# Performance work log

Measured on AMD Instinct MI355X. Metric: run time of the kernel, lower is better.

## Reference

```python
import jax, jax.numpy as jnp
import numpy as np

TEMPERATURE = 0.07
BASE_TEMPERATURE = 0.07


def setup_inputs() -> dict:
    key = jax.random.key(0)
    k1, k2 = jax.random.split(key)
    N, D = 8192, 512
    features = jax.random.normal(k1, (N, D), dtype=jnp.float32)
    labels = jax.random.randint(k2, (N,), 0, 64, dtype=jnp.int64 if jax.config.jax_enable_x64 else jnp.int32)
    return {"features": features, "labels": labels, "rotation_multiplier": 2}


def reference(features, labels, rotation_multiplier):
    k = int(rotation_multiplier)
    N = features.shape[0]
    B = N // k
    # L2-normalize rows (torch F.normalize clamps norm at eps=1e-12)
    norm = jnp.maximum(jnp.linalg.norm(features, axis=1, keepdims=True), 1e-12)
    f = features / norm
    sim = jnp.matmul(f, f.T) / TEMPERATURE  # [N, N]

    # block positive mask: groups of k rows share a label; compare group labels
    lab = labels.reshape(B, k)[:, 0]  # [B]
    same = lab[:, None] == lab[None, :]  # [B, B]
    mask = jnp.repeat(jnp.repeat(same, k, axis=0), k, axis=1)  # [N, N]
    eye = jnp.eye(N, dtype=bool)
    mask = mask & ~eye

    # stable masked log-softmax with diagonal removed from denominator
    logits_max = jax.lax.stop_gradient(jnp.max(sim, axis=1, keepdims=True))
    logits = sim - logits_max
    exp_logits = jnp.exp(logits)
    denom = exp_logits.sum(axis=1, keepdims=True) - jnp.diagonal(exp_logits)[:, None] + 1e-8
    log_prob = logits - jnp.log(denom)

    mask_f = mask.astype(logits.dtype)
    mask_sum = mask_f.sum(axis=1)  # [N]
    valid = mask_sum > 0
    mean_log_prob_pos = (log_prob * mask_f).sum(axis=1) / jnp.maximum(mask_sum, 1.0)
    per_sample = -(TEMPERATURE / BASE_TEMPERATURE) * mean_log_prob_pos
    n_valid = valid.sum().astype(logits.dtype)
    loss = jnp.where(valid, per_sample, 0.0).sum() / jnp.maximum(n_valid, 1.0)
    return loss
```

## Files before the change

kernel.cpp:

```cpp
#include <hip/hip_runtime.h>
#include <hip/hip_bf16.h>

#define TEMP_INV 14.285714285714286f
#define FSCALE 16.0f
#define T1S (TEMP_INV / 256.0f)

typedef __attribute__((ext_vector_type(4))) float f32x4;
typedef __attribute__((ext_vector_type(4))) int i32x4;
typedef __attribute__((ext_vector_type(8))) int i32x8;

#define ASYNC_COPY16(gp, lp)                                                  \
  __builtin_amdgcn_global_load_lds(                                          \
      (__attribute__((address_space(1))) const void*)(gp),                    \
      (__attribute__((address_space(3))) void*)(lp), 16, 0, 0)

__global__ __launch_bounds__(256) void norm_label_k(const float* __restrict__ feat,
                                                    uchar* __restrict__ fq,
                                                    const int* __restrict__ labels,
                                                    const int* __restrict__ kptr,
                                                    int* __restrict__ glab,
                                                    int* __restrict__ cnt,
                                                    float* __restrict__ gacc,
                                                    int* __restrict__ dcnt,
                                                    int N, int D) {
  const int row = (blockIdx.x * 256 + threadIdx.x) >> 6;
  const int lane = threadIdx.x & 63;
  if (row < N) {
    const float4* fr = (const float4*)(feat + (size_t)row * D);
    float4 v0 = fr[lane * 2];
    float4 v1 = fr[lane * 2 + 1];
    float ss = v0.x * v0.x + v0.y * v0.y + v0.z * v0.z + v0.w * v0.w +
               v1.x * v1.x + v1.y * v1.y + v1.z * v1.z + v1.w * v1.w;
    #pragma unroll
    for (int off = 32; off; off >>= 1) ss += __shfl_xor(ss, off, 64);
    const float inv = FSCALE / fmaxf(sqrtf(ss), 1e-12f);
    int w0 = 0, w1 = 0;
    w0 = __builtin_amdgcn_cvt_pk_fp8_f32(v0.x * inv, v0.y * inv, w0, false);
    w0 = __builtin_amdgcn_cvt_pk_fp8_f32(v0.z * inv, v0.w * inv, w0, true);
    w1 = __builtin_amdgcn_cvt_pk_fp8_f32(v1.x * inv, v1.y * inv, w1, false);
    w1 = __builtin_amdgcn_cvt_pk_fp8_f32(v1.z * inv, v1.w * inv, w1, true);
    uint2 o; o.x = (uint)w0; o.y = (uint)w1;
    const int pofs = (lane >> 4) * 128 + (lane & 3) * 32 + ((lane >> 2) & 3) * 8;
    *(uint2*)(fq + (size_t)row * D + pofs) = o;
  }
  if (blockIdx.x == 0) {
    const int k = *kptr;
    const int B = N / k;
    __shared__ int h[64];
    const int t = threadIdx.x;
    if (t < 2) gacc[t] = 0.f;
    if (t == 2) *dcnt = 0;
    if (t < 64) h[t] = 0;
    __syncthreads();
    for (int b = t; b < B; b += 256) {
      int lb = labels[(size_t)b * k];
      if (lb >= 0 && lb < 64) atomicAdd(&h[lb], 1);
    }
    __syncthreads();
    if (t < 64) cnt[t] = h[t];
    for (int i = t; i < N; i += 256) glab[i] = labels[(size_t)(i / k) * k];
  }
}

__global__ __launch_bounds__(256, 4) void gemm_k(const uchar* __restrict__ fq,
                                                 const int* __restrict__ glab,
                                                 float* __restrict__ part,
                                                 int N, int D) {
  __shared__ uchar As[128 * 128];
  __shared__ uchar Bs[128 * 128];
  const int t = threadIdx.x;
  const int lane = t & 63;
  const int wid = t >> 6;
  const int wrow = wid >> 1, wcol = wid & 1;
  const int quad = lane >> 4, l15 = lane & 15;

  const int nb = N / 128;
  const int total = nb * (nb + 1) / 2;
  int gidx = blockIdx.x;
  if ((total & 7) == 0) {
    const int per = total >> 3;
    gidx = (blockIdx.x & 7) * per + (blockIdx.x >> 3);
  }
  int idx = gidx, bi = 0;
  while (idx >= nb - bi) { idx -= nb - bi; bi++; }
  const int bj = bi + idx;
  const int i0 = bi * 128, j0 = bj * 128;
  const bool diagblk = (bi == bj);

  f32x4 acc[4][4];
  #pragma unroll
  for (int mi = 0; mi < 4; mi++)
    #pragma unroll
    for (int ni = 0; ni < 4; ni++) {
      f32x4 z = {0.f, 0.f, 0.f, 0.f};
      acc[mi][ni] = z;
    }

  uchar* sb = (wid < 2) ? As : Bs;
  const int rbase = (wid & 1) * 64;
  const int rowstart = ((wid < 2) ? i0 : j0) + rbase;
  const int lrow = lane >> 3;
  const int lch = lane & 7;

  for (int kb = 0; kb < D; kb += 128) {
    __syncthreads();
    #pragma unroll
    for (int i = 0; i < 8; i++) {
      const int rl = 8 * i + lrow;
      const int cg = lch ^ (rl & 7);
      ASYNC_COPY16(fq + (size_t)(rowstart + rl) * D + kb + cg * 16,
                   sb + (rbase + 8 * i) * 128);
    }
    __syncthreads();
    i32x8 av[4];
    #pragma unroll
    for (int mi = 0; mi < 4; mi++) {
      const int r = wrow * 64 + mi * 16 + l15;
      i32x4 lo = *(const i32x4*)&As[r * 128 + (((2 * quad) ^ (r & 7)) << 4)];
      i32x4 hi = *(const i32x4*)&As[r * 128 + (((2 * quad + 1) ^ (r & 7)) << 4)];
      av[mi] = (i32x8){lo.x, lo.y, lo.z, lo.w, hi.x, hi.y, hi.z, hi.w};
    }
    #pragma unroll
    for (int ni = 0; ni < 4; ni++) {
      const int r = wcol * 64 + ni * 16 + l15;
      i32x4 lo = *(const i32x4*)&Bs[r * 128 + (((2 * quad) ^ (r & 7)) << 4)];
      i32x4 hi = *(const i32x4*)&Bs[r * 128 + (((2 * quad + 1) ^ (r & 7)) << 4)];
      i32x8 bv = (i32x8){lo.x, lo.y, lo.z, lo.w, hi.x, hi.y, hi.z, hi.w};
      #pragma unroll
      for (int mi = 0; mi < 4; mi++)
        acc[mi][ni] = __builtin_amdgcn_mfma_scale_f32_16x16x128_f8f6f4(
            av[mi], bv, acc[mi][ni], 0, 0, 0, 127, 0, 127);
    }
  }

  __syncthreads();
  float* sf = (float*)As;
  const int colbase = j0 + wcol * 64 + l15;
  int clab[4];
  #pragma unroll
  for (int ni = 0; ni < 4; ni++) clab[ni] = glab[colbase + ni * 16];

  float colE[4] = {0.f, 0.f, 0.f, 0.f};
  float colP[4] = {0.f, 0.f, 0.f, 0.f};

  #pragma unroll
  for (int mi = 0; mi < 4; mi++) {
    const int lrw = wrow * 64 + mi * 16 + quad * 4;
    #pragma unroll
    for (int r = 0; r < 4; r++) {
      const int row = i0 + lrw + r;
      const int rlab = glab[row];
      float Ssum = 0.f, Psum = 0.f;
      #pragma unroll
      for (int ni = 0; ni < 4; ni++) {
        const int col = colbase + ni * 16;
        const float val = acc[mi][ni][r];
        const float lg = fmaf(val, T1S, -TEMP_INV);
        const bool diag = diagblk && (row == col);
        const float e = diag ? 0.f : __expf(lg);
        const float pm = (!diag && rlab == clab[ni]) ? lg : 0.f;
        Ssum += e; Psum += pm;
        colE[ni] += e; colP[ni] += pm;
      }
      #pragma unroll
      for (int off = 8; off; off >>= 1) {
        Ssum += __shfl_xor(Ssum, off, 64);
        Psum += __shfl_xor(Psum, off, 64);
      }
      if (l15 == 0) {
        sf[wcol * 128 + lrw + r]       = Ssum;
        sf[256 + wcol * 128 + lrw + r] = Psum;
      }
    }
  }
  if (!diagblk) {
    #pragma unroll
    for (int ni = 0; ni < 4; ni++) {
      float e = colE[ni];
      float p = colP[ni];
      e += __shfl_xor(e, 16, 64);
      e += __shfl_xor(e, 32, 64);
      p += __shfl_xor(p, 16, 64);
      p += __shfl_xor(p, 32, 64);
      const int lcol = wcol * 64 + ni * 16 + l15;
      if (quad == 0) {
        sf[512 + wrow * 128 + lcol] = e;
        sf[768 + wrow * 128 + lcol] = p;
      }
    }
  }
  __syncthreads();
  float* dst = part + (size_t)gidx * 512;
  if (t < 128) {
    dst[t]       = sf[t] + sf[128 + t];
    dst[128 + t] = sf[256 + t] + sf[384 + t];
  } else if (!diagblk) {
    const int u = t - 128;
    dst[256 + u] = sf[512 + u] + sf[640 + u];
    dst[384 + u] = sf[768 + u] + sf[896 + u];
  }
}

__global__ __launch_bounds__(512) void reduce_loss_k(const float* __restrict__ part,
                                                     const int* __restrict__ glab,
                                                     const int* __restrict__ cnt,
                                                     const int* __restrict__ kptr,
                                                     float* __restrict__ gacc,
                                                     int* __restrict__ dcnt,
                                                     float* __restrict__ out, int N) {
  const int nb = N / 128;
  const int b = blockIdx.x;
  const int t = threadIdx.x & 127;
  const int sl = threadIdx.x >> 7;
  float S = 0.f, P = 0.f;
  const int base = b * nb - b * (b - 1) / 2;
  for (int bj = b + sl; bj < nb; bj += 4) {
    const float* p = part + (size_t)(base + bj - b) * 512;
    S += p[t];
    P += p[128 + t];
  }
  for (int bi = sl; bi < b; bi += 4) {
    const int idx = bi * nb - bi * (bi - 1) / 2 + (b - bi);
    const float* p = part + (size_t)idx * 512;
    S += p[256 + t];
    P += p[384 + t];
  }
  __shared__ float sS[4][128], sP[4][128];
  sS[sl][t] = S; sP[sl][t] = P;
  __syncthreads();
  float l = 0.f, v = 0.f;
  if (sl == 0) {
    S = sS[0][t] + sS[1][t] + sS[2][t] + sS[3][t];
    P = sP[0][t] + sP[1][t] + sP[2][t] + sP[3][t];
    const int k = *kptr;
    const int np = cnt[glab[b * 128 + t]] * k - 1;
    if (np > 0) {
      l = -(P - (float)np * logf(S + 1e-8f)) / (float)np;
      v = 1.f;
    }
  }
  #pragma unroll
  for (int off = 32; off; off >>= 1) {
    l += __shfl_xor(l, off, 64);
    v += __shfl_xor(v, off, 64);
  }
  __shared__ float sl8[8], sv8[8];
  const int tt = threadIdx.x;
  if ((tt & 63) == 0) { sl8[tt >> 6] = l; sv8[tt >> 6] = v; }
  __syncthreads();
  if (tt == 0) {
    float L = 0.f, V = 0.f;
    #pragma unroll
    for (int i = 0; i < 8; i++) { L += sl8[i]; V += sv8[i]; }
    atomicAdd(&gacc[0], L);
    atomicAdd(&gacc[1], V);
    __threadfence();
    const int prev = atomicAdd(dcnt, 1);
    if (prev == (int)gridDim.x - 1) {
      const float Lf = atomicAdd(&gacc[0], 0.f);
      const float Vf = atomicAdd(&gacc[1], 0.f);
      out[0] = Lf / fmaxf(Vf, 1.f);
    }
  }
}

extern "C" void kernel_launch(void* const* d_in, const int* in_sizes, int n_in,
                              void* d_out, int out_size, void* d_ws, size_t ws_size,
                              hipStream_t stream) {
  const float* feat = (const float*)d_in[0];
  const int* labels = (const int*)d_in[1];
  const int* kptr   = (const int*)d_in[2];
  const int N = in_sizes[1];
  const int D = in_sizes[0] / N;

  const int nb = N / 128;
  const int total = nb * (nb + 1) / 2;

  char* ws = (char*)d_ws;
  uchar* fq = (uchar*)ws;
  size_t off = (size_t)N * D;
  float* part = (float*)(ws + off); off += (size_t)total * 512 * sizeof(float);
  int* glab   = (int*)(ws + off);   off += (size_t)N * sizeof(int);
  int* cnt    = (int*)(ws + off);   off += 64 * sizeof(int);
  float* gacc = (float*)(ws + off); off += 2 * sizeof(float);
  int* dcnt   = (int*)(ws + off);   off += sizeof(int);

  norm_label_k<<<(N + 3) / 4, 256, 0, stream>>>(feat, fq, labels, kptr, glab, cnt,
                                                gacc, dcnt, N, D);
  gemm_k<<<total, 256, 0, stream>>>(fq, glab, part, N, D);
  reduce_loss_k<<<nb, 512, 0, stream>>>(part, glab, cnt, kptr, gacc, dcnt,
                                        (float*)d_out, N);
}
```

Before: 135.8 us.

## Move label histogram into reduce kernel and widen reduce blocks

Block 0 of the normalize kernel no longer serially computes the label histogram and the full group-label array. Each row's group label is now written by its own wave, and the 64-bin histogram is recomputed per block inside the reduce kernel in shared memory. The reduce kernel also grows to 1024 threads with 8 slices over the partial tiles. This removes a straggler block from the first kernel at the cost of redundant histogram work in every reduce block.

```diff
diff --git a/kernel.cpp b/kernel.cpp
--- a/kernel.cpp
+++ b/kernel.cpp
@@ -14,15 +14,14 @@
       (__attribute__((address_space(1))) const void*)(gp),                    \
       (__attribute__((address_space(3))) void*)(lp), 16, 0, 0)
 
-__global__ __launch_bounds__(256) void norm_label_k(const float* __restrict__ feat,
-                                                    uchar* __restrict__ fq,
-                                                    const int* __restrict__ labels,
-                                                    const int* __restrict__ kptr,
-                                                    int* __restrict__ glab,
-                                                    int* __restrict__ cnt,
-                                                    float* __restrict__ gacc,
-                                                    int* __restrict__ dcnt,
-                                                    int N, int D) {
+__global__ __launch_bounds__(256) void norm_k(const float* __restrict__ feat,
+                                              uchar* __restrict__ fq,
+                                              const int* __restrict__ labels,
+                                              const int* __restrict__ kptr,
+                                              int* __restrict__ glab,
+                                              float* __restrict__ gacc,
+                                              int* __restrict__ dcnt,
+                                              int N, int D) {
   const int row = (blockIdx.x * 256 + threadIdx.x) >> 6;
   const int lane = threadIdx.x & 63;
   if (row < N) {
@@ -42,23 +41,14 @@
     uint2 o; o.x = (uint)w0; o.y = (uint)w1;
     const int pofs = (lane >> 4) * 128 + (lane & 3) * 32 + ((lane >> 2) & 3) * 8;
     *(uint2*)(fq + (size_t)row * D + pofs) = o;
-  }
-  if (blockIdx.x == 0) {
-    const int k = *kptr;
-    const int B = N / k;
-    __shared__ int h[64];
-    const int t = threadIdx.x;
-    if (t < 2) gacc[t] = 0.f;
-    if (t == 2) *dcnt = 0;
-    if (t < 64) h[t] = 0;
-    __syncthreads();
-    for (int b = t; b < B; b += 256) {
-      int lb = labels[(size_t)b * k];
-      if (lb >= 0 && lb < 64) atomicAdd(&h[lb], 1);
-    }
-    __syncthreads();
-    if (t < 64) cnt[t] = h[t];
-    for (int i = t; i < N; i += 256) glab[i] = labels[(size_t)(i / k) * k];
+    if (lane == 0) {
+      const int k = *kptr;
+      glab[row] = labels[(size_t)(row / k) * k];
+    }
+  }
+  if (blockIdx.x == 0 && threadIdx.x < 3) {
+    if (threadIdx.x < 2) gacc[threadIdx.x] = 0.f;
+    else *dcnt = 0;
   }
 }
 
@@ -201,39 +191,51 @@
   }
 }
 
-__global__ __launch_bounds__(512) void reduce_loss_k(const float* __restrict__ part,
-                                                     const int* __restrict__ glab,
-                                                     const int* __restrict__ cnt,
-                                                     const int* __restrict__ kptr,
-                                                     float* __restrict__ gacc,
-                                                     int* __restrict__ dcnt,
-                                                     float* __restrict__ out, int N) {
+__global__ __launch_bounds__(1024) void reduce_loss_k(const float* __restrict__ part,
+                                                      const int* __restrict__ glab,
+                                                      const int* __restrict__ labels,
+                                                      const int* __restrict__ kptr,
+                                                      float* __restrict__ gacc,
+                                                      int* __restrict__ dcnt,
+                                                      float* __restrict__ out, int N) {
   const int nb = N / 128;
   const int b = blockIdx.x;
-  const int t = threadIdx.x & 127;
-  const int sl = threadIdx.x >> 7;
+  const int tt = threadIdx.x;
+  const int t = tt & 127;
+  const int sl = tt >> 7;
+  const int k = *kptr;
+  const int B = N / k;
+
+  __shared__ int h[64];
+  if (tt < 64) h[tt] = 0;
+  __syncthreads();
+  for (int g = tt; g < B; g += 1024) {
+    int lb = labels[(size_t)g * k];
+    if (lb >= 0 && lb < 64) atomicAdd(&h[lb], 1);
+  }
+
   float S = 0.f, P = 0.f;
   const int base = b * nb - b * (b - 1) / 2;
-  for (int bj = b + sl; bj < nb; bj += 4) {
+  for (int bj = b + sl; bj < nb; bj += 8) {
     const float* p = part + (size_t)(base + bj - b) * 512;
     S += p[t];
     P += p[128 + t];
   }
-  for (int bi = sl; bi < b; bi += 4) {
+  for (int bi = sl; bi < b; bi += 8) {
     const int idx = bi * nb - bi * (bi - 1) / 2 + (b - bi);
     const float* p = part + (size_t)idx * 512;
     S += p[256 + t];
     P += p[384 + t];
   }
-  __shared__ float sS[4][128], sP[4][128];
+  __shared__ float sS[8][128], sP[8][128];
   sS[sl][t] = S; sP[sl][t] = P;
   __syncthreads();
   float l = 0.f, v = 0.f;
   if (sl == 0) {
-    S = sS[0][t] + sS[1][t] + sS[2][t] + sS[3][t];
-    P = sP[0][t] + sP[1][t] + sP[2][t] + sP[3][t];
-    const int k = *kptr;
-    const int np = cnt[glab[b * 128 + t]] * k - 1;
+    S = 0.f; P = 0.f;
+    #pragma unroll
+    for (int s = 0; s < 8; s++) { S += sS[s][t]; P += sP[s][t]; }
+    const int np = h[glab[b * 128 + t]] * k - 1;
     if (np > 0) {
       l = -(P - (float)np * logf(S + 1e-8f)) / (float)np;
       v = 1.f;
@@ -244,14 +246,13 @@
     l += __shfl_xor(l, off, 64);
     v += __shfl_xor(v, off, 64);
   }
-  __shared__ float sl8[8], sv8[8];
-  const int tt = threadIdx.x;
-  if ((tt & 63) == 0) { sl8[tt >> 6] = l; sv8[tt >> 6] = v; }
+  __shared__ float sl16[16], sv16[16];
+  if ((tt & 63) == 0) { sl16[tt >> 6] = l; sv16[tt >> 6] = v; }
   __syncthreads();
   if (tt == 0) {
     float L = 0.f, V = 0.f;
     #pragma unroll
-    for (int i = 0; i < 8; i++) { L += sl8[i]; V += sv8[i]; }
+    for (int i = 0; i < 16; i++) { L += sl16[i]; V += sv16[i]; }
     atomicAdd(&gacc[0], L);
     atomicAdd(&gacc[1], V);
     __threadfence();
@@ -281,13 +282,12 @@
   size_t off = (size_t)N * D;
   float* part = (float*)(ws + off); off += (size_t)total * 512 * sizeof(float);
   int* glab   = (int*)(ws + off);   off += (size_t)N * sizeof(int);
-  int* cnt    = (int*)(ws + off);   off += 64 * sizeof(int);
   float* gacc = (float*)(ws + off); off += 2 * sizeof(float);
   int* dcnt   = (int*)(ws + off);   off += sizeof(int);
 
-  norm_label_k<<<(N + 3) / 4, 256, 0, stream>>>(feat, fq, labels, kptr, glab, cnt,
-                                                gacc, dcnt, N, D);
+  norm_k<<<(N + 3) / 4, 256, 0, stream>>>(feat, fq, labels, kptr, glab,
+                                          gacc, dcnt, N, D);
   gemm_k<<<total, 256, 0, stream>>>(fq, glab, part, N, D);
-  reduce_loss_k<<<nb, 512, 0, stream>>>(part, glab, cnt, kptr, gacc, dcnt,
-                                        (float*)d_out, N);
-}
+  reduce_loss_k<<<nb, 1024, 0, stream>>>(part, glab, labels, kptr, gacc, dcnt,
+                                         (float*)d_out, N);
+}
```

Result: faster. 129.3 us, median of 2 (-4.8%).
